# Performance work log

Measured on AMD Instinct MI355X. Metric: run time of the kernel, lower is better.

Reference implementation:

```python
import jax, jax.numpy as jnp
import numpy as np

H = 1024
V = 50257


def setup_inputs() -> dict:
    key = jax.random.key(0)
    ks = jax.random.split(key, 10)
    s = 0.02
    return {
        "x": jax.random.randint(ks[0], (1,), 0, V, dtype=jnp.int32),
        "h0": jax.random.normal(ks[1], (1, 1, H), jnp.float32),
        "c0": jax.random.normal(ks[2], (1, 1, H), jnp.float32),
        "emb": jax.random.normal(ks[3], (V, H), jnp.float32) * s,
        "w_ih": jax.random.normal(ks[4], (4 * H, H), jnp.float32) * s,
        "w_hh": jax.random.normal(ks[5], (4 * H, H), jnp.float32) * s,
        "b_ih": jax.random.normal(ks[6], (4 * H,), jnp.float32) * s,
        "b_hh": jax.random.normal(ks[7], (4 * H,), jnp.float32) * s,
        "w_out": jax.random.normal(ks[8], (V, H), jnp.float32) * s,
        "b_out": jax.random.normal(ks[9], (V,), jnp.float32) * s,
    }


def reference(x, h0, c0, emb, w_ih, w_hh, b_ih, b_hh, w_out, b_out):
    # embedding lookup + view(1,1,-1) + relu -> [1, H]
    e = jax.nn.relu(emb[x].reshape(1, H))
    h = h0[0]  # [1, H]
    c = c0[0]  # [1, H]
    # single LSTM cell step; PyTorch gate order: i, f, g, o
    gates = e @ w_ih.T + b_ih + h @ w_hh.T + b_hh  # [1, 4H]
    i, f, g, o = jnp.split(gates, 4, axis=1)
    c_new = jax.nn.sigmoid(f) * c + jax.nn.sigmoid(i) * jnp.tanh(g)
    h_new = jax.nn.sigmoid(o) * jnp.tanh(c_new)
    # output projection + log-softmax over vocab
    logits = h_new @ w_out.T + b_out  # [1, V]
    out = jax.nn.log_softmax(logits, axis=1)
    return out, (h_new[None, :, :], c_new[None, :, :])
```

## Files before the change

### kernel.cpp

```cpp
#include <hip/hip_runtime.h>
#include <math.h>

#define HH 1024
#define VV 50257
#define NLB 2048
#define NWAVE (NLB * 4)
#define TBASE (6 * NWAVE)

__device__ __forceinline__ void lse_comb(float& m, float& s, float om, float os) {
    float M = fmaxf(m, om);
    s = s * __expf(m - M) + os * __expf(om - M);
    m = M;
}

__device__ __forceinline__ float sigmoidf(float x) { return 1.0f / (1.0f + __expf(-x)); }

__device__ __forceinline__ float dot4(float4 a, float4 b) {
    return a.x * b.x + a.y * b.y + a.z * b.z + a.w * b.w;
}

__global__ __launch_bounds__(512) void k_gatecell(
    const int* __restrict__ x, const float* __restrict__ emb,
    const float* __restrict__ h0, const float* __restrict__ c0,
    const float* __restrict__ w_ih, const float* __restrict__ w_hh,
    const float* __restrict__ b_ih, const float* __restrict__ b_hh,
    float* __restrict__ out) {
    __shared__ float sg2[8];
    const int j = blockIdx.x;
    const int w = threadIdx.x >> 6;
    const int lane = threadIdx.x & 63;
    const int g = w >> 1, hf = w & 1;
    const int row = g * HH + j;
    const int base = hf * 512 + lane * 8;

    const float* e  = emb + (size_t)x[0] * HH + base;
    const float* wi = w_ih + (size_t)row * HH + base;
    const float* wh = w_hh + (size_t)row * HH + base;
    const float* hp = h0 + base;

    float4 wi0 = *reinterpret_cast<const float4*>(wi);
    float4 wi1 = *reinterpret_cast<const float4*>(wi + 4);
    float4 wh0 = *reinterpret_cast<const float4*>(wh);
    float4 wh1 = *reinterpret_cast<const float4*>(wh + 4);
    float4 e0  = *reinterpret_cast<const float4*>(e);
    float4 e1  = *reinterpret_cast<const float4*>(e + 4);
    float4 hv0 = *reinterpret_cast<const float4*>(hp);
    float4 hv1 = *reinterpret_cast<const float4*>(hp + 4);
    e0.x = fmaxf(e0.x, 0.f); e0.y = fmaxf(e0.y, 0.f);
    e0.z = fmaxf(e0.z, 0.f); e0.w = fmaxf(e0.w, 0.f);
    e1.x = fmaxf(e1.x, 0.f); e1.y = fmaxf(e1.y, 0.f);
    e1.z = fmaxf(e1.z, 0.f); e1.w = fmaxf(e1.w, 0.f);

    float acc = dot4(wi0, e0) + dot4(wi1, e1) + dot4(wh0, hv0) + dot4(wh1, hv1);
#pragma unroll
    for (int off = 1; off < 64; off <<= 1) acc += __shfl_xor(acc, off, 64);
    if (lane == 0)
        sg2[w] = acc + (hf == 0 ? b_ih[row] + b_hh[row] : 0.0f);
    __syncthreads();
    if (threadIdx.x == 0) {
        float ig = sigmoidf(sg2[0] + sg2[1]);
        float fg = sigmoidf(sg2[2] + sg2[3]);
        float gg = tanhf(sg2[4] + sg2[5]);
        float og = sigmoidf(sg2[6] + sg2[7]);
        float c = fg * c0[j] + ig * gg;
        float h = og * tanhf(c);
        out[VV + j] = h;
        out[VV + HH + j] = c;
    }
}

__global__ __launch_bounds__(256, 8) void k_logits_lse(
    const float* __restrict__ w_out, const float* __restrict__ b_out,
    const float* __restrict__ h, float* __restrict__ logits,
    float* __restrict__ pm, float* __restrict__ ps) {
    __shared__ float4 hs4[256];
    __shared__ float sm[4], ss[4];
    const int tid = threadIdx.x;
    const int w = tid >> 6;
    const int lane = tid & 63;
    const int halfid = lane >> 5;
    const int hl = lane & 31;

    hs4[tid] = reinterpret_cast<const float4*>(h)[tid];
    __syncthreads();

    const int wid = blockIdx.x * 4 + w;
    float m = -1e30f, s = 0.0f;

#pragma unroll
    for (int k = 0; k < 3; ++k) {
        const int r = wid + (2 * k + halfid) * NWAVE;
        const float* p = w_out + (size_t)r * HH + hl * 4;
        float acc = 0.0f;
#pragma unroll
        for (int j = 0; j < 8; ++j) {
            float4 wv = *reinterpret_cast<const float4*>(p + j * 128);
            acc += dot4(wv, hs4[hl + 32 * j]);
        }
#pragma unroll
        for (int off = 1; off < 32; off <<= 1) acc += __shfl_xor(acc, off, 64);
        const float v = acc + b_out[r];
        if (hl == 0) logits[r] = v;
        float M = fmaxf(m, v);
        s = s * __expf(m - M) + __expf(v - M);
        m = M;
    }
    if (wid <= 552) {
        const int r = TBASE + 2 * wid + halfid;
        const bool valid = (r < VV);
        const int rc = valid ? r : (VV - 1);
        const float* p = w_out + (size_t)rc * HH + hl * 4;
        float acc = 0.0f;
#pragma unroll
        for (int j = 0; j < 8; ++j) {
            float4 wv = *reinterpret_cast<const float4*>(p + j * 128);
            acc += dot4(wv, hs4[hl + 32 * j]);
        }
#pragma unroll
        for (int off = 1; off < 32; off <<= 1) acc += __shfl_xor(acc, off, 64);
        float v = valid ? (acc + b_out[rc]) : -1e30f;
        if (hl == 0 && valid) logits[r] = v;
        float M = fmaxf(m, v);
        s = s * __expf(m - M) + __expf(v - M);
        m = M;
    }

    {
        float om = __shfl_xor(m, 32, 64);
        float os = __shfl_xor(s, 32, 64);
        lse_comb(m, s, om, os);
    }
    if (lane == 0) { sm[w] = m; ss[w] = s; }
    __syncthreads();
    if (tid == 0) {
        float M = sm[0], S = ss[0];
#pragma unroll
        for (int q = 1; q < 4; ++q) lse_comb(M, S, sm[q], ss[q]);
        pm[blockIdx.x] = M;
        ps[blockIdx.x] = S;
    }
}

__global__ __launch_bounds__(256) void k_final(
    const float* __restrict__ logits, const float* __restrict__ pm,
    const float* __restrict__ ps, float* __restrict__ out) {
    __shared__ float sm[4], ss[4];
    __shared__ float sZ;
    int tid = threadIdx.x;
    int lane = tid & 63;
    float m = -1e30f, s = 0.0f;
#pragma unroll
    for (int t = 0; t < NLB / 256; ++t) {
        int p = tid + t * 256;
        lse_comb(m, s, pm[p], ps[p]);
    }
#pragma unroll
    for (int off = 1; off < 64; off <<= 1) {
        float om = __shfl_xor(m, off, 64);
        float os = __shfl_xor(s, off, 64);
        lse_comb(m, s, om, os);
    }
    if (lane == 0) { sm[tid >> 6] = m; ss[tid >> 6] = s; }
    __syncthreads();
    if (tid == 0) {
        float M = sm[0], S = ss[0];
#pragma unroll
        for (int q = 1; q < 4; ++q) lse_comb(M, S, sm[q], ss[q]);
        sZ = M + logf(S);
    }
    __syncthreads();
    float Z = sZ;
    for (int i = blockIdx.x * 256 + tid; i < VV; i += gridDim.x * 256)
        out[i] = logits[i] - Z;
}

extern "C" void kernel_launch(void* const* d_in, const int* in_sizes, int n_in,
                              void* d_out, int out_size, void* d_ws, size_t ws_size,
                              hipStream_t stream) {
    const int*   x     = (const int*)d_in[0];
    const float* h0    = (const float*)d_in[1];
    const float* c0    = (const float*)d_in[2];
    const float* emb   = (const float*)d_in[3];
    const float* w_ih  = (const float*)d_in[4];
    const float* w_hh  = (const float*)d_in[5];
    const float* b_ih  = (const float*)d_in[6];
    const float* b_hh  = (const float*)d_in[7];
    const float* w_out = (const float*)d_in[8];
    const float* b_out = (const float*)d_in[9];
    float* out = (float*)d_out;
    float* ws  = (float*)d_ws;

    float* logits = ws;
    float* pm     = ws + 50304;
    float* ps     = pm + NLB;

    k_gatecell<<<HH, 512, 0, stream>>>(x, emb, h0, c0, w_ih, w_hh, b_ih, b_hh, out);
    k_logits_lse<<<NLB, 256, 0, stream>>>(w_out, b_out, out + VV, logits, pm, ps);
    k_final<<<256, 256, 0, stream>>>(logits, pm, ps, out);
}
```

Measured before the change: 46.37 us.

## Fuse LSTM cell and logits kernels with grid barrier and LDS prefetch

Merges the gate/cell kernel and the logits+LSE kernel into one persistent-style launch of 1024 blocks. A software grid barrier (atomic counter plus spin) makes every block wait until all h values exist. While the gate computation runs, each wave prefetches its first w_out row into LDS with global_load_lds, overlapping that load with the LSTM phase. The aim is to remove one kernel launch boundary and hide part of the w_out stream. In exchange it adds a memset, spin-wait overhead, and a deadlock risk if the 1024 blocks cannot all be resident at once.

```diff
diff --git a/kernel.cpp b/kernel.cpp
--- a/kernel.cpp
+++ b/kernel.cpp
@@ -3,100 +3,125 @@
 
 #define HH 1024
 #define VV 50257
-#define NLB 2048
-#define NWAVE (NLB * 4)
-#define TBASE (6 * NWAVE)
+#define NBLK 1024
+#define NW (NBLK * 8)
+#define TB (6 * NW)
+#define NTL (VV - TB)
 
 __device__ __forceinline__ void lse_comb(float& m, float& s, float om, float os) {
     float M = fmaxf(m, om);
     s = s * __expf(m - M) + os * __expf(om - M);
     m = M;
 }
-
 __device__ __forceinline__ float sigmoidf(float x) { return 1.0f / (1.0f + __expf(-x)); }
-
 __device__ __forceinline__ float dot4(float4 a, float4 b) {
     return a.x * b.x + a.y * b.y + a.z * b.z + a.w * b.w;
 }
 
-__global__ __launch_bounds__(512) void k_gatecell(
+__global__ __launch_bounds__(512, 8) void k_fused(
     const int* __restrict__ x, const float* __restrict__ emb,
     const float* __restrict__ h0, const float* __restrict__ c0,
     const float* __restrict__ w_ih, const float* __restrict__ w_hh,
     const float* __restrict__ b_ih, const float* __restrict__ b_hh,
-    float* __restrict__ out) {
-    __shared__ float sg2[8];
+    const float* __restrict__ w_out, const float* __restrict__ b_out,
+    float* __restrict__ out, float* __restrict__ hbuf,
+    float* __restrict__ logits, float* __restrict__ pm, float* __restrict__ ps,
+    unsigned int* __restrict__ ctr) {
+    __shared__ float4 pre[2048];
+    __shared__ float4 hs4[256];
+    __shared__ float sg2[8], sm[8], ss[8];
+    const int tid = threadIdx.x;
+    const int w = tid >> 6;
+    const int lane = tid & 63;
     const int j = blockIdx.x;
-    const int w = threadIdx.x >> 6;
-    const int lane = threadIdx.x & 63;
-    const int g = w >> 1, hf = w & 1;
-    const int row = g * HH + j;
-    const int base = hf * 512 + lane * 8;
-
-    const float* e  = emb + (size_t)x[0] * HH + base;
-    const float* wi = w_ih + (size_t)row * HH + base;
-    const float* wh = w_hh + (size_t)row * HH + base;
-    const float* hp = h0 + base;
-
-    float4 wi0 = *reinterpret_cast<const float4*>(wi);
-    float4 wi1 = *reinterpret_cast<const float4*>(wi + 4);
-    float4 wh0 = *reinterpret_cast<const float4*>(wh);
-    float4 wh1 = *reinterpret_cast<const float4*>(wh + 4);
-    float4 e0  = *reinterpret_cast<const float4*>(e);
-    float4 e1  = *reinterpret_cast<const float4*>(e + 4);
-    float4 hv0 = *reinterpret_cast<const float4*>(hp);
-    float4 hv1 = *reinterpret_cast<const float4*>(hp + 4);
-    e0.x = fmaxf(e0.x, 0.f); e0.y = fmaxf(e0.y, 0.f);
-    e0.z = fmaxf(e0.z, 0.f); e0.w = fmaxf(e0.w, 0.f);
-    e1.x = fmaxf(e1.x, 0.f); e1.y = fmaxf(e1.y, 0.f);
-    e1.z = fmaxf(e1.z, 0.f); e1.w = fmaxf(e1.w, 0.f);
-
-    float acc = dot4(wi0, e0) + dot4(wi1, e1) + dot4(wh0, hv0) + dot4(wh1, hv1);
-#pragma unroll
-    for (int off = 1; off < 64; off <<= 1) acc += __shfl_xor(acc, off, 64);
-    if (lane == 0)
-        sg2[w] = acc + (hf == 0 ? b_ih[row] + b_hh[row] : 0.0f);
-    __syncthreads();
-    if (threadIdx.x == 0) {
+    const int widl = blockIdx.x * 8 + w;
+
+    {
+        const float* prow = w_out + (size_t)widl * HH;
+#pragma unroll
+        for (int i = 0; i < 4; ++i) {
+            auto* gsrc = (const __attribute__((address_space(1))) unsigned int*)
+                             (const void*)(prow + i * 256 + lane * 4);
+            auto* ldst = (__attribute__((address_space(3))) unsigned int*)
+                             (void*)(&pre[w * 256 + i * 64]);
+            __builtin_amdgcn_global_load_lds(gsrc, ldst, 16, 0, 0);
+        }
+    }
+
+    {
+        const int g = w >> 1, hf = w & 1;
+        const int row = g * HH + j;
+        const int base = hf * 512 + lane * 8;
+        const float* e  = emb + (size_t)x[0] * HH + base;
+        const float* wi = w_ih + (size_t)row * HH + base;
+        const float* wh = w_hh + (size_t)row * HH + base;
+        const float* hp = h0 + base;
+        float4 wi0 = *reinterpret_cast<const float4*>(wi);
+        float4 wi1 = *reinterpret_cast<const float4*>(wi + 4);
+        float4 wh0 = *reinterpret_cast<const float4*>(wh);
+        float4 wh1 = *reinterpret_cast<const float4*>(wh + 4);
+        float4 e0  = *reinterpret_cast<const float4*>(e);
+        float4 e1  = *reinterpret_cast<const float4*>(e + 4);
+        float4 hv0 = *reinterpret_cast<const float4*>(hp);
+        float4 hv1 = *reinterpret_cast<const float4*>(hp + 4);
+        e0.x = fmaxf(e0.x, 0.f); e0.y = fmaxf(e0.y, 0.f);
+        e0.z = fmaxf(e0.z, 0.f); e0.w = fmaxf(e0.w, 0.f);
+        e1.x = fmaxf(e1.x, 0.f); e1.y = fmaxf(e1.y, 0.f);
+        e1.z = fmaxf(e1.z, 0.f); e1.w = fmaxf(e1.w, 0.f);
+        float acc = dot4(wi0, e0) + dot4(wi1, e1) + dot4(wh0, hv0) + dot4(wh1, hv1);
+#pragma unroll
+        for (int off = 1; off < 64; off <<= 1) acc += __shfl_xor(acc, off, 64);
+        if (lane == 0)
+            sg2[w] = acc + (hf == 0 ? b_ih[row] + b_hh[row] : 0.0f);
+    }
+    __syncthreads();
+    if (tid == 0) {
         float ig = sigmoidf(sg2[0] + sg2[1]);
         float fg = sigmoidf(sg2[2] + sg2[3]);
         float gg = tanhf(sg2[4] + sg2[5]);
         float og = sigmoidf(sg2[6] + sg2[7]);
         float c = fg * c0[j] + ig * gg;
         float h = og * tanhf(c);
+        hbuf[j] = h;
         out[VV + j] = h;
         out[VV + HH + j] = c;
-    }
-}
-
-__global__ __launch_bounds__(256, 8) void k_logits_lse(
-    const float* __restrict__ w_out, const float* __restrict__ b_out,
-    const float* __restrict__ h, float* __restrict__ logits,
-    float* __restrict__ pm, float* __restrict__ ps) {
-    __shared__ float4 hs4[256];
-    __shared__ float sm[4], ss[4];
-    const int tid = threadIdx.x;
-    const int w = tid >> 6;
-    const int lane = tid & 63;
+        __threadfence();
+        __hip_atomic_fetch_add(ctr, 1u, __ATOMIC_RELEASE, __HIP_MEMORY_SCOPE_AGENT);
+        while (__hip_atomic_load(ctr, __ATOMIC_RELAXED, __HIP_MEMORY_SCOPE_AGENT) < (unsigned)NBLK)
+            __builtin_amdgcn_s_sleep(8);
+        (void)__hip_atomic_load(ctr, __ATOMIC_ACQUIRE, __HIP_MEMORY_SCOPE_AGENT);
+    }
+    __syncthreads();
+    if (tid < 256) hs4[tid] = reinterpret_cast<const float4*>(hbuf)[tid];
+    __syncthreads();
+
     const int halfid = lane >> 5;
     const int hl = lane & 31;
-
-    hs4[tid] = reinterpret_cast<const float4*>(h)[tid];
-    __syncthreads();
-
-    const int wid = blockIdx.x * 4 + w;
     float m = -1e30f, s = 0.0f;
-
-#pragma unroll
-    for (int k = 0; k < 3; ++k) {
-        const int r = wid + (2 * k + halfid) * NWAVE;
+    asm volatile("s_waitcnt vmcnt(0)" ::: "memory");
+
+    {
+        float acc = 0.0f;
+#pragma unroll
+        for (int i = 0; i < 4; ++i)
+            acc += dot4(pre[w * 256 + lane + 64 * i], hs4[lane + 64 * i]);
+#pragma unroll
+        for (int off = 1; off < 64; off <<= 1) acc += __shfl_xor(acc, off, 64);
+        float v = acc + b_out[widl];
+        if (lane == 0) logits[widl] = v;
+        float vv = halfid ? -1e30f : v;
+        float M = fmaxf(m, vv);
+        s = s * __expf(m - M) + __expf(vv - M);
+        m = M;
+    }
+#pragma unroll
+    for (int k = 0; k < 2; ++k) {
+        const int r = widl + (1 + 2 * k + halfid) * NW;
         const float* p = w_out + (size_t)r * HH + hl * 4;
         float acc = 0.0f;
 #pragma unroll
-        for (int j = 0; j < 8; ++j) {
-            float4 wv = *reinterpret_cast<const float4*>(p + j * 128);
-            acc += dot4(wv, hs4[hl + 32 * j]);
-        }
+        for (int jj = 0; jj < 8; ++jj)
+            acc += dot4(*reinterpret_cast<const float4*>(p + jj * 128), hs4[hl + 32 * jj]);
 #pragma unroll
         for (int off = 1; off < 32; off <<= 1) acc += __shfl_xor(acc, off, 64);
         const float v = acc + b_out[r];
@@ -105,23 +130,36 @@
         s = s * __expf(m - M) + __expf(v - M);
         m = M;
     }
-    if (wid <= 552) {
-        const int r = TBASE + 2 * wid + halfid;
-        const bool valid = (r < VV);
-        const int rc = valid ? r : (VV - 1);
-        const float* p = w_out + (size_t)rc * HH + hl * 4;
-        float acc = 0.0f;
-#pragma unroll
-        for (int j = 0; j < 8; ++j) {
-            float4 wv = *reinterpret_cast<const float4*>(p + j * 128);
-            acc += dot4(wv, hs4[hl + 32 * j]);
-        }
-#pragma unroll
-        for (int off = 1; off < 32; off <<= 1) acc += __shfl_xor(acc, off, 64);
-        float v = valid ? (acc + b_out[rc]) : -1e30f;
-        if (hl == 0 && valid) logits[r] = v;
-        float M = fmaxf(m, v);
-        s = s * __expf(m - M) + __expf(v - M);
+    {
+        const int r = widl + 5 * NW;
+        const float* p = w_out + (size_t)r * HH + lane * 4;
+        float acc = 0.0f;
+#pragma unroll
+        for (int i = 0; i < 4; ++i)
+            acc += dot4(*reinterpret_cast<const float4*>(p + i * 256), hs4[lane + 64 * i]);
+#pragma unroll
+        for (int off = 1; off < 64; off <<= 1) acc += __shfl_xor(acc, off, 64);
+        float v = acc + b_out[r];
+        if (lane == 0) logits[r] = v;
+        float vv = halfid ? -1e30f : v;
+        float M = fmaxf(m, vv);
+        s = s * __expf(m - M) + __expf(vv - M);
+        m = M;
+    }
+    if (widl < NTL) {
+        const int r = TB + widl;
+        const float* p = w_out + (size_t)r * HH + lane * 4;
+        float acc = 0.0f;
+#pragma unroll
+        for (int i = 0; i < 4; ++i)
+            acc += dot4(*reinterpret_cast<const float4*>(p + i * 256), hs4[lane + 64 * i]);
+#pragma unroll
+        for (int off = 1; off < 64; off <<= 1) acc += __shfl_xor(acc, off, 64);
+        float v = acc + b_out[r];
+        if (lane == 0) logits[r] = v;
+        float vv = halfid ? -1e30f : v;
+        float M = fmaxf(m, vv);
+        s = s * __expf(m - M) + __expf(vv - M);
         m = M;
     }
 
@@ -135,7 +173,7 @@
     if (tid == 0) {
         float M = sm[0], S = ss[0];
 #pragma unroll
-        for (int q = 1; q < 4; ++q) lse_comb(M, S, sm[q], ss[q]);
+        for (int q = 1; q < 8; ++q) lse_comb(M, S, sm[q], ss[q]);
         pm[blockIdx.x] = M;
         ps[blockIdx.x] = S;
     }
@@ -150,7 +188,7 @@
     int lane = tid & 63;
     float m = -1e30f, s = 0.0f;
 #pragma unroll
-    for (int t = 0; t < NLB / 256; ++t) {
+    for (int t = 0; t < NBLK / 256; ++t) {
         int p = tid + t * 256;
         lse_comb(m, s, pm[p], ps[p]);
     }
@@ -190,11 +228,14 @@
     float* out = (float*)d_out;
     float* ws  = (float*)d_ws;
 
-    float* logits = ws;
-    float* pm     = ws + 50304;
-    float* ps     = pm + NLB;
-
-    k_gatecell<<<HH, 512, 0, stream>>>(x, emb, h0, c0, w_ih, w_hh, b_ih, b_hh, out);
-    k_logits_lse<<<NLB, 256, 0, stream>>>(w_out, b_out, out + VV, logits, pm, ps);
+    float* hbuf   = ws;
+    float* logits = ws + 1024;
+    float* pm     = ws + 1024 + 50304;
+    float* ps     = pm + NBLK;
+    unsigned int* ctr = (unsigned int*)(ps + NBLK);
+
+    hipMemsetAsync(ctr, 0, sizeof(unsigned int), stream);
+    k_fused<<<NBLK, 512, 0, stream>>>(x, emb, h0, c0, w_ih, w_hh, b_ih, b_hh,
+                                      w_out, b_out, out, hbuf, logits, pm, ps, ctr);
     k_final<<<256, 256, 0, stream>>>(logits, pm, ps, out);
 }
```

Measured after the change: 178.6 us. 285% more time.
